# Kernel optimization log

Measured on AMD Instinct MI355X. Metric: run time of the kernel, lower is better.

The kernel has to match this reference:

```python
import jax, jax.numpy as jnp
import numpy as np

B, S, D, E, K = 4, 2048, 768, 8, 2


def setup_inputs() -> dict:
    key = jax.random.key(0)
    ks = jax.random.split(key, 5)
    s = 0.02
    return {
        "x": jax.random.normal(ks[0], (B, S, D), dtype=jnp.float32),
        "gate_w": jax.random.normal(ks[1], (D, E), dtype=jnp.float32) * s,
        "gate_b": jnp.zeros((E,), dtype=jnp.float32),
        "w1": jax.random.normal(ks[2], (E, D, D), dtype=jnp.float32) * s,
        "b1": jnp.zeros((E, D), dtype=jnp.float32),
        "w2": jax.random.normal(ks[3], (E, D, D), dtype=jnp.float32) * s,
        "b2": jnp.zeros((E, D), dtype=jnp.float32),
    }


def reference(x, gate_w, gate_b, w1, b1, w2, b2):
    # MoE forward, eval mode (no gate noise, dropout = identity)
    b, s, d = x.shape
    xf = x.reshape(-1, d)                                  # [T, D]
    T = xf.shape[0]

    gate_logits = xf @ gate_w + gate_b                     # [T, E]
    gate_scores = jax.nn.softmax(gate_logits, axis=-1)

    topv, topi = jax.lax.top_k(gate_scores, K)             # [T, K]
    topv = topv / (jnp.sum(topv, axis=-1, keepdims=True) + 1e-8)

    # scatter top-k weights into dense per-expert combine weights [T, E]
    comb = jnp.zeros((T, E), dtype=xf.dtype).at[
        jnp.arange(T)[:, None], topi].add(topv)

    # expert MLPs (dense over experts; combine weights zero-out unselected)
    h = jax.nn.relu(jnp.einsum('td,edh->teh', xf, w1) + b1)  # [T, E, D]
    y = jnp.einsum('teh,eho->teo', h, w2) + b2               # [T, E, D]
    out = jnp.einsum('te,teo->to', comb, y).reshape(b, s, -1)

    # load-balance aux loss (CV^2 of expert importance)
    importance = gate_scores.sum(axis=0)                   # [E]
    cv2 = importance.var() / (importance.mean() ** 2 + 1e-8)
    aux_loss = 0.01 * cv2
    return out, aux_loss
```

## Files before the change

kernel.cpp:

```cpp
#include <hip/hip_runtime.h>


#define T_TOK 8192
#define D_DIM 768
#define E_EXP 8
#define TK    16384
#define MAXCHUNK 136

typedef __attribute__((ext_vector_type(4))) float f32x4;
typedef __attribute__((ext_vector_type(8))) short s16x8;
typedef __attribute__((ext_vector_type(8))) unsigned short u16x8;

static __device__ __forceinline__ unsigned short f2bf(float f) {
    union { float f; unsigned u; } v; v.f = f;
    unsigned r = v.u + 0x7FFFu + ((v.u >> 16) & 1u);
    return (unsigned short)(r >> 16);
}
static __device__ __forceinline__ float bf2f(unsigned short h) {
    union { unsigned u; float f; } v; v.u = ((unsigned)h) << 16;
    return v.f;
}

static __device__ __forceinline__ void gload_lds16(const unsigned short* g, unsigned short* l) {
    __builtin_amdgcn_global_load_lds(
        (const __attribute__((address_space(1))) unsigned int*)(const void*)g,
        (__attribute__((address_space(3))) unsigned int*)(void*)l,
        16, 0, 0);
}

__global__ __launch_bounds__(256) void gate_kernel(
    const float* __restrict__ x, const float* __restrict__ gw,
    const float* __restrict__ gb, unsigned short* __restrict__ xb,
    int* __restrict__ ea, int* __restrict__ eb,
    float* __restrict__ wa, float* __restrict__ wb,
    int* __restrict__ counts, float* __restrict__ importance,
    int* __restrict__ basep, int* __restrict__ cursor,
    int* __restrict__ done, float* __restrict__ aux_out,
    int* __restrict__ nchunks, int* __restrict__ c2e, int* __restrict__ c2m)
{
    __shared__ float s_imp[4][8];
    __shared__ int   s_cnt[4][8];
    const int tid = threadIdx.x, wid = tid >> 6, lane = tid & 63;
    const int wg = blockIdx.x * 4 + wid;

    float imp[8]; int cnt[8];
    #pragma unroll
    for (int e = 0; e < 8; ++e) { imp[e] = 0.f; cnt[e] = 0; }

    for (int i = 0; i < 8; ++i) {
        const int t = wg + i * 1024;
        const float* xr = x + (size_t)t * D_DIM;
        float xv[12];
        float acc[8];
        #pragma unroll
        for (int e = 0; e < 8; ++e) acc[e] = 0.f;
        #pragma unroll
        for (int j = 0; j < 12; ++j) {
            const int d = lane + j * 64;
            float v = xr[d];
            xv[j] = v;
            xb[(size_t)t * D_DIM + d] = f2bf(v);
        }
        #pragma unroll
        for (int j = 0; j < 12; ++j) {
            const int d = lane + j * 64;
            const f32x4* g = (const f32x4*)(gw + (size_t)d * 8);
            f32x4 g0 = g[0], g1 = g[1];
            float v = xv[j];
            acc[0] += v * g0[0]; acc[1] += v * g0[1];
            acc[2] += v * g0[2]; acc[3] += v * g0[3];
            acc[4] += v * g1[0]; acc[5] += v * g1[1];
            acc[6] += v * g1[2]; acc[7] += v * g1[3];
        }
        #pragma unroll
        for (int s = 1; s < 64; s <<= 1) {
            #pragma unroll
            for (int e = 0; e < 8; ++e) acc[e] += __shfl_xor(acc[e], s);
        }
        float lg[8], mx = -1e30f;
        #pragma unroll
        for (int e = 0; e < 8; ++e) { lg[e] = acc[e] + gb[e]; mx = fmaxf(mx, lg[e]); }
        float p[8], ssum = 0.f;
        #pragma unroll
        for (int e = 0; e < 8; ++e) { p[e] = expf(lg[e] - mx); ssum += p[e]; }
        float sc[8];
        float inv_s = 1.f / ssum;
        #pragma unroll
        for (int e = 0; e < 8; ++e) { sc[e] = p[e] * inv_s; imp[e] += sc[e]; }
        float v0 = sc[0], v1 = -1e30f;
        int   i0 = 0,     i1 = -1;
        #pragma unroll
        for (int e = 1; e < 8; ++e) {
            if (sc[e] > v0)      { v1 = v0; i1 = i0; v0 = sc[e]; i0 = e; }
            else if (sc[e] > v1) { v1 = sc[e]; i1 = e; }
        }
        #pragma unroll
        for (int e = 0; e < 8; ++e) cnt[e] += (e == i0 ? 1 : 0) + (e == i1 ? 1 : 0);
        float inv = 1.f / (v0 + v1 + 1e-8f);
        if (lane == 0) {
            ea[t] = i0; eb[t] = i1; wa[t] = v0 * inv; wb[t] = v1 * inv;
        }
    }
    if (lane == 0) {
        #pragma unroll
        for (int e = 0; e < 8; ++e) { s_imp[wid][e] = imp[e]; s_cnt[wid][e] = cnt[e]; }
    }
    __syncthreads();
    if (tid < 8) {
        float si = 0.f; int sc2 = 0;
        #pragma unroll
        for (int w = 0; w < 4; ++w) { si += s_imp[w][tid]; sc2 += s_cnt[w][tid]; }
        atomicAdd(importance + tid, si);
        atomicAdd(counts + tid, sc2);
    }
    __threadfence();
    __syncthreads();
    if (tid == 0) {
        if (atomicAdd(done, 1) == (int)gridDim.x - 1) {
            int c[8]; float im[8];
            #pragma unroll
            for (int e = 0; e < 8; ++e) {
                c[e]  = atomicAdd(counts + e, 0);
                im[e] = atomicAdd(importance + e, 0.0f);
            }
            int b = 0, nc = 0;
            #pragma unroll
            for (int e = 0; e < 8; ++e) {
                basep[e] = b; cursor[e] = b;
                for (int m = 0; m < c[e]; m += 128) { c2e[nc] = e; c2m[nc] = m; ++nc; }
                b += c[e];
            }
            nchunks[0] = nc;
            float mean = 0.f;
            #pragma unroll
            for (int e = 0; e < 8; ++e) mean += im[e];
            mean *= 0.125f;
            float var = 0.f;
            #pragma unroll
            for (int e = 0; e < 8; ++e) { float d = im[e] - mean; var += d * d; }
            var *= 0.125f;
            aux_out[0] = 0.01f * var / (mean * mean + 1e-8f);
        }
    }
}

__global__ __launch_bounds__(256) void scatter_kernel(
    const int* __restrict__ ea, const int* __restrict__ eb,
    const float* __restrict__ wa, const float* __restrict__ wb,
    int* __restrict__ cursor, int* __restrict__ list,
    float* __restrict__ wgt, int* __restrict__ slot)
{
    const int t = blockIdx.x * 256 + threadIdx.x;
    const int lane = threadIdx.x & 63;
    #pragma unroll
    for (int k = 0; k < 2; ++k) {
        const int e = k ? eb[t] : ea[t];
        const float w = k ? wb[t] : wa[t];
        int pos = 0;
        for (int ex = 0; ex < 8; ++ex) {
            unsigned long long m = __ballot(e == ex);
            if (e == ex) {
                int leader = __ffsll((unsigned long long)m) - 1;
                int n = __popcll(m);
                int p0 = 0;
                if (lane == leader) p0 = atomicAdd(cursor + ex, n);
                p0 = __shfl(p0, leader);
                pos = p0 + __popcll(m & ((1ull << lane) - 1ull));
            }
        }
        list[pos] = t; wgt[pos] = w; slot[t * 2 + k] = pos;
    }
}

__global__ __launch_bounds__(256) void tconv_kernel(
    const float* __restrict__ w1, const float* __restrict__ w2,
    unsigned short* __restrict__ w1t, unsigned short* __restrict__ w2t)
{
    const int z = blockIdx.z;
    const float* src = (z < 8 ? w1 : w2) + (size_t)(z & 7) * D_DIM * D_DIM;
    unsigned short* dst = (z < 8 ? w1t : w2t) + (size_t)(z & 7) * D_DIM * D_DIM;
    __shared__ float tile[32][33];
    const int tx = threadIdx.x, ty = threadIdx.y;
    const int k0 = blockIdx.x * 32, n0 = blockIdx.y * 32;
    #pragma unroll
    for (int j = 0; j < 4; ++j)
        tile[ty + j * 8][tx] = src[(size_t)(k0 + ty + j * 8) * D_DIM + n0 + tx];
    __syncthreads();
    #pragma unroll
    for (int j = 0; j < 4; ++j)
        dst[(size_t)(n0 + ty + j * 8) * D_DIM + k0 + tx] = f2bf(tile[tx][ty + j * 8]);
}

template<int GATHER, int RELU>
__global__ __launch_bounds__(256) void moe_gemm_kernel(
    const unsigned short* __restrict__ A, const unsigned short* __restrict__ Bt,
    const float* __restrict__ bias, unsigned short* __restrict__ C,
    const int* __restrict__ counts, const int* __restrict__ basep,
    const int* __restrict__ list,
    const int* __restrict__ nchunks, const int* __restrict__ c2e,
    const int* __restrict__ c2m)
{
    const int cid = blockIdx.x;
    if (cid >= nchunks[0]) return;
    const int e = c2e[cid];
    const int m0 = c2m[cid];
    const int count = counts[e];
    const int n0 = blockIdx.y * 128;
    const int base = basep[e];

    constexpr int NT = D_DIM / 32;
    constexpr int LB = 128 * 32;

    __shared__ unsigned short Al[3 * LB];
    __shared__ unsigned short Bl[3 * LB];

    const int tid = threadIdx.x;
    const int lane = tid & 63, wid = tid >> 6;
    const int wr = wid >> 1, wc = wid & 1;

    const int sr = wid * 16 + (lane >> 2);
    const int sc = (lane & 3) * 8;

    int r0 = m0 + sr;      if (r0 >= count) r0 = count - 1;
    int r1 = m0 + 64 + sr; if (r1 >= count) r1 = count - 1;
    const size_t t0 = GATHER ? (size_t)list[base + r0] : (size_t)(base + r0);
    const size_t t1 = GATHER ? (size_t)list[base + r1] : (size_t)(base + r1);
    const unsigned short* gA0 = A + t0 * D_DIM + sc;
    const unsigned short* gA1 = A + t1 * D_DIM + sc;
    const unsigned short* gB0 = Bt + ((size_t)e * D_DIM + n0 + sr) * D_DIM + sc;
    const unsigned short* gB1 = Bt + ((size_t)e * D_DIM + n0 + 64 + sr) * D_DIM + sc;
    const int lds0 = (wid * 16) * 32;
    const int lds1 = (64 + wid * 16) * 32;

    f32x4 acc[4][4];
    #pragma unroll
    for (int mi = 0; mi < 4; ++mi)
        #pragma unroll
        for (int ni = 0; ni < 4; ++ni)
            acc[mi][ni] = (f32x4)(0.f);

#define STAGE(kt, bi) do {                                   \
        const int _k = (kt) * 32;                            \
        gload_lds16(gA0 + _k, Al + (bi) * LB + lds0);        \
        gload_lds16(gA1 + _k, Al + (bi) * LB + lds1);        \
        gload_lds16(gB0 + _k, Bl + (bi) * LB + lds0);        \
        gload_lds16(gB1 + _k, Bl + (bi) * LB + lds1);        \
    } while (0)

    STAGE(0, 0);
    STAGE(1, 1);
    asm volatile("s_waitcnt vmcnt(4)" ::: "memory");
    __builtin_amdgcn_s_barrier();
    __builtin_amdgcn_sched_barrier(0);

    #pragma unroll
    for (int t = 0; t < NT; ++t) {
        const int cb = t % 3;
        const int sb = (t + 2) % 3;
        if (t + 2 < NT) STAGE(t + 2, sb);

        s16x8 af[4], bfr[4];
        #pragma unroll
        for (int mi = 0; mi < 4; ++mi)
            af[mi] = *(const s16x8*)&Al[cb * LB + (wr * 64 + mi * 16 + (lane & 15)) * 32 + (lane >> 4) * 8];
        #pragma unroll
        for (int ni = 0; ni < 4; ++ni)
            bfr[ni] = *(const s16x8*)&Bl[cb * LB + (wc * 64 + ni * 16 + (lane & 15)) * 32 + (lane >> 4) * 8];
        #pragma unroll
        for (int mi = 0; mi < 4; ++mi)
            #pragma unroll
            for (int ni = 0; ni < 4; ++ni)
                acc[mi][ni] = __builtin_amdgcn_mfma_f32_16x16x32_bf16(
                    af[mi], bfr[ni], acc[mi][ni], 0, 0, 0);

        __builtin_amdgcn_sched_barrier(0);
        if (t + 2 < NT) { asm volatile("s_waitcnt vmcnt(4)" ::: "memory"); }
        else            { asm volatile("s_waitcnt vmcnt(0)" ::: "memory"); }
        __builtin_amdgcn_s_barrier();
        __builtin_amdgcn_sched_barrier(0);
    }
#undef STAGE

    #pragma unroll
    for (int ni = 0; ni < 4; ++ni) {
        const int cn = n0 + wc * 64 + ni * 16 + (lane & 15);
        const float bv = bias[e * D_DIM + cn];
        #pragma unroll
        for (int mi = 0; mi < 4; ++mi) {
            #pragma unroll
            for (int j = 0; j < 4; ++j) {
                const int rm = m0 + wr * 64 + mi * 16 + (lane >> 4) * 4 + j;
                if (rm < count) {
                    float v = acc[mi][ni][j] + bv;
                    if (RELU) v = fmaxf(v, 0.f);
                    C[(size_t)(base + rm) * D_DIM + cn] = f2bf(v);
                }
            }
        }
    }
}

__global__ __launch_bounds__(256) void combine_kernel(
    const unsigned short* __restrict__ y, const int* __restrict__ slot,
    const float* __restrict__ wgt, float* __restrict__ out)
{
    const int g = blockIdx.x * 256 + threadIdx.x;
    const int t = g / 96;
    const int n = (g % 96) * 8;
    const int s0 = slot[t * 2], s1 = slot[t * 2 + 1];
    const float w0 = wgt[s0], w1 = wgt[s1];
    u16x8 ya = *(const u16x8*)(y + (size_t)s0 * D_DIM + n);
    u16x8 yb = *(const u16x8*)(y + (size_t)s1 * D_DIM + n);
    f32x4 o0, o1;
    #pragma unroll
    for (int i = 0; i < 4; ++i) o0[i] = w0 * bf2f(ya[i])     + w1 * bf2f(yb[i]);
    #pragma unroll
    for (int i = 0; i < 4; ++i) o1[i] = w0 * bf2f(ya[4 + i]) + w1 * bf2f(yb[4 + i]);
    float* op = out + (size_t)t * D_DIM + n;
    *(f32x4*)op       = o0;
    *(f32x4*)(op + 4) = o1;
}

extern "C" void kernel_launch(void* const* d_in, const int* in_sizes, int n_in,
                              void* d_out, int out_size, void* d_ws, size_t ws_size,
                              hipStream_t stream)
{
    const float* x  = (const float*)d_in[0];
    const float* gw = (const float*)d_in[1];
    const float* gb = (const float*)d_in[2];
    const float* w1 = (const float*)d_in[3];
    const float* b1 = (const float*)d_in[4];
    const float* w2 = (const float*)d_in[5];
    const float* b2 = (const float*)d_in[6];
    float* out = (float*)d_out;

    char* ws = (char*)d_ws;
    size_t off = 0;
    auto alloc = [&](size_t bytes) {
        char* p = ws + off; off += (bytes + 255) & ~(size_t)255; return p;
    };
    unsigned short* xb  = (unsigned short*)alloc((size_t)T_TOK * D_DIM * 2);
    unsigned short* w1t = (unsigned short*)alloc((size_t)E_EXP * D_DIM * D_DIM * 2);
    unsigned short* w2t = (unsigned short*)alloc((size_t)E_EXP * D_DIM * D_DIM * 2);
    unsigned short* h   = (unsigned short*)alloc((size_t)TK * D_DIM * 2);
    unsigned short* y   = (unsigned short*)alloc((size_t)TK * D_DIM * 2);
    int*   list = (int*)alloc(TK * 4);
    float* wgt  = (float*)alloc(TK * 4);
    int*   slot = (int*)alloc(TK * 4);
    int*   ea   = (int*)alloc(T_TOK * 4);
    int*   eb   = (int*)alloc(T_TOK * 4);
    float* wa   = (float*)alloc(T_TOK * 4);
    float* wb   = (float*)alloc(T_TOK * 4);
    int*   meta = (int*)alloc(2048);
    int*   counts  = meta;
    int*   basep   = meta + 8;
    int*   cursor  = meta + 16;
    int*   done    = meta + 24;
    int*   nchunks = meta + 25;
    float* importance = (float*)(meta + 26);
    int*   c2e     = meta + 34;
    int*   c2m     = meta + 34 + MAXCHUNK;

    hipMemsetAsync(meta, 0, 2048, stream);
    tconv_kernel<<<dim3(24, 24, 16), dim3(32, 8), 0, stream>>>(w1, w2, w1t, w2t);
    gate_kernel<<<256, 256, 0, stream>>>(x, gw, gb, xb, ea, eb, wa, wb, counts, importance,
                                         basep, cursor, done, out + (out_size - 1),
                                         nchunks, c2e, c2m);
    scatter_kernel<<<32, 256, 0, stream>>>(ea, eb, wa, wb, cursor, list, wgt, slot);
    moe_gemm_kernel<1, 1><<<dim3(MAXCHUNK, 6), 256, 0, stream>>>(xb, w1t, b1, h, counts, basep, list,
                                                                 nchunks, c2e, c2m);
    moe_gemm_kernel<0, 0><<<dim3(MAXCHUNK, 6), 256, 0, stream>>>(h, w2t, b2, y, counts, basep, list,
                                                                 nchunks, c2e, c2m);
    combine_kernel<<<3072, 256, 0, stream>>>(y, slot, wgt, out);
}
```

Measured before the change: 296.2 us.

## Enlarge MoE GEMM M-tile to 256 with swizzled LDS and double gate grid

The expert GEMM tile grows from 128x128 to 256x128 rows per block. Each wave now holds 8x4 accumulators, and the chunk size and chunk count change to match. LDS reads use an XOR swizzle on the k-chunk to reduce bank conflicts, and the final-iteration barrier is dropped. The gate kernel launches twice as many blocks with fewer tokens each, for more parallelism. The larger tile roughly doubles accumulator register pressure (launch bounds ask for 2 blocks/SM) and leaves fewer blocks in the grid, with more padding waste on partial chunks.

```diff
diff --git a/kernel.cpp b/kernel.cpp
--- a/kernel.cpp
+++ b/kernel.cpp
@@ -5,7 +5,7 @@
 #define D_DIM 768
 #define E_EXP 8
 #define TK    16384
-#define MAXCHUNK 136
+#define MAXCHUNK 72
 
 typedef __attribute__((ext_vector_type(4))) float f32x4;
 typedef __attribute__((ext_vector_type(8))) short s16x8;
@@ -47,8 +47,8 @@
     #pragma unroll
     for (int e = 0; e < 8; ++e) { imp[e] = 0.f; cnt[e] = 0; }
 
-    for (int i = 0; i < 8; ++i) {
-        const int t = wg + i * 1024;
+    for (int i = 0; i < 4; ++i) {
+        const int t = wg + i * 2048;
         const float* xr = x + (size_t)t * D_DIM;
         float xv[12];
         float acc[8];
@@ -127,7 +127,7 @@
             #pragma unroll
             for (int e = 0; e < 8; ++e) {
                 basep[e] = b; cursor[e] = b;
-                for (int m = 0; m < c[e]; m += 128) { c2e[nc] = e; c2m[nc] = m; ++nc; }
+                for (int m = 0; m < c[e]; m += 256) { c2e[nc] = e; c2m[nc] = m; ++nc; }
                 b += c[e];
             }
             nchunks[0] = nc;
@@ -192,7 +192,7 @@
 }
 
 template<int GATHER, int RELU>
-__global__ __launch_bounds__(256) void moe_gemm_kernel(
+__global__ __launch_bounds__(256, 2) void moe_gemm_kernel(
     const unsigned short* __restrict__ A, const unsigned short* __restrict__ Bt,
     const float* __restrict__ bias, unsigned short* __restrict__ C,
     const int* __restrict__ counts, const int* __restrict__ basep,
@@ -208,88 +208,99 @@
     const int n0 = blockIdx.y * 128;
     const int base = basep[e];
 
-    constexpr int NT = D_DIM / 32;
-    constexpr int LB = 128 * 32;
-
-    __shared__ unsigned short Al[3 * LB];
-    __shared__ unsigned short Bl[3 * LB];
+    constexpr int NT  = D_DIM / 32;
+    constexpr int ALB = 256 * 32;
+    constexpr int BLB = 128 * 32;
+
+    __shared__ unsigned short Al[3 * ALB];
+    __shared__ unsigned short Bl[3 * BLB];
 
     const int tid = threadIdx.x;
     const int lane = tid & 63, wid = tid >> 6;
     const int wr = wid >> 1, wc = wid & 1;
 
-    const int sr = wid * 16 + (lane >> 2);
-    const int sc = (lane & 3) * 8;
-
-    int r0 = m0 + sr;      if (r0 >= count) r0 = count - 1;
-    int r1 = m0 + 64 + sr; if (r1 >= count) r1 = count - 1;
-    const size_t t0 = GATHER ? (size_t)list[base + r0] : (size_t)(base + r0);
-    const size_t t1 = GATHER ? (size_t)list[base + r1] : (size_t)(base + r1);
-    const unsigned short* gA0 = A + t0 * D_DIM + sc;
-    const unsigned short* gA1 = A + t1 * D_DIM + sc;
-    const unsigned short* gB0 = Bt + ((size_t)e * D_DIM + n0 + sr) * D_DIM + sc;
-    const unsigned short* gB1 = Bt + ((size_t)e * D_DIM + n0 + 64 + sr) * D_DIM + sc;
-    const int lds0 = (wid * 16) * 32;
-    const int lds1 = (64 + wid * 16) * 32;
-
-    f32x4 acc[4][4];
-    #pragma unroll
-    for (int mi = 0; mi < 4; ++mi)
+    const int ro  = lane >> 2;
+    const int sch = ((lane & 3) ^ (ro & 3)) * 8;
+
+    const unsigned short *gA0, *gA1, *gA2, *gA3, *gB0, *gB1;
+    {
+        int r, row;
+        row = wid * 64 + 0 * 16 + ro; r = m0 + row; if (r >= count) r = count - 1;
+        gA0 = A + (GATHER ? (size_t)list[base + r] : (size_t)(base + r)) * D_DIM + sch;
+        row = wid * 64 + 1 * 16 + ro; r = m0 + row; if (r >= count) r = count - 1;
+        gA1 = A + (GATHER ? (size_t)list[base + r] : (size_t)(base + r)) * D_DIM + sch;
+        row = wid * 64 + 2 * 16 + ro; r = m0 + row; if (r >= count) r = count - 1;
+        gA2 = A + (GATHER ? (size_t)list[base + r] : (size_t)(base + r)) * D_DIM + sch;
+        row = wid * 64 + 3 * 16 + ro; r = m0 + row; if (r >= count) r = count - 1;
+        gA3 = A + (GATHER ? (size_t)list[base + r] : (size_t)(base + r)) * D_DIM + sch;
+        gB0 = Bt + ((size_t)e * D_DIM + n0 + wid * 32 + 0 * 16 + ro) * D_DIM + sch;
+        gB1 = Bt + ((size_t)e * D_DIM + n0 + wid * 32 + 1 * 16 + ro) * D_DIM + sch;
+    }
+    const int lA0 = (wid * 64 +  0) * 32, lA1 = (wid * 64 + 16) * 32;
+    const int lA2 = (wid * 64 + 32) * 32, lA3 = (wid * 64 + 48) * 32;
+    const int lB0 = (wid * 32 +  0) * 32, lB1 = (wid * 32 + 16) * 32;
+
+#define STAGE(kt, bi) do {                                      \
+        gload_lds16(gA0 + (kt) * 32, Al + (bi) * ALB + lA0);    \
+        gload_lds16(gA1 + (kt) * 32, Al + (bi) * ALB + lA1);    \
+        gload_lds16(gA2 + (kt) * 32, Al + (bi) * ALB + lA2);    \
+        gload_lds16(gA3 + (kt) * 32, Al + (bi) * ALB + lA3);    \
+        gload_lds16(gB0 + (kt) * 32, Bl + (bi) * BLB + lB0);    \
+        gload_lds16(gB1 + (kt) * 32, Bl + (bi) * BLB + lB1);    \
+    } while (0)
+
+    f32x4 acc[8][4];
+    #pragma unroll
+    for (int mi = 0; mi < 8; ++mi)
         #pragma unroll
         for (int ni = 0; ni < 4; ++ni)
             acc[mi][ni] = (f32x4)(0.f);
 
-#define STAGE(kt, bi) do {                                   \
-        const int _k = (kt) * 32;                            \
-        gload_lds16(gA0 + _k, Al + (bi) * LB + lds0);        \
-        gload_lds16(gA1 + _k, Al + (bi) * LB + lds1);        \
-        gload_lds16(gB0 + _k, Bl + (bi) * LB + lds0);        \
-        gload_lds16(gB1 + _k, Bl + (bi) * LB + lds1);        \
-    } while (0)
+    const int sw8 = (((lane >> 4) ^ (lane & 3)) * 8);
+    const int l15 = lane & 15;
 
     STAGE(0, 0);
     STAGE(1, 1);
-    asm volatile("s_waitcnt vmcnt(4)" ::: "memory");
+    asm volatile("s_waitcnt vmcnt(6)" ::: "memory");
     __builtin_amdgcn_s_barrier();
     __builtin_amdgcn_sched_barrier(0);
 
     #pragma unroll
     for (int t = 0; t < NT; ++t) {
         const int cb = t % 3;
-        const int sb = (t + 2) % 3;
-        if (t + 2 < NT) STAGE(t + 2, sb);
-
-        s16x8 af[4], bfr[4];
-        #pragma unroll
-        for (int mi = 0; mi < 4; ++mi)
-            af[mi] = *(const s16x8*)&Al[cb * LB + (wr * 64 + mi * 16 + (lane & 15)) * 32 + (lane >> 4) * 8];
+        if (t + 2 < NT) STAGE(t + 2, (t + 2) % 3);
+
+        s16x8 af[8], bfr[4];
+        #pragma unroll
+        for (int mi = 0; mi < 8; ++mi)
+            af[mi] = *(const s16x8*)&Al[cb * ALB + (wr * 128 + mi * 16 + l15) * 32 + sw8];
         #pragma unroll
         for (int ni = 0; ni < 4; ++ni)
-            bfr[ni] = *(const s16x8*)&Bl[cb * LB + (wc * 64 + ni * 16 + (lane & 15)) * 32 + (lane >> 4) * 8];
-        #pragma unroll
-        for (int mi = 0; mi < 4; ++mi)
+            bfr[ni] = *(const s16x8*)&Bl[cb * BLB + (wc * 64 + ni * 16 + l15) * 32 + sw8];
+        #pragma unroll
+        for (int mi = 0; mi < 8; ++mi)
             #pragma unroll
             for (int ni = 0; ni < 4; ++ni)
                 acc[mi][ni] = __builtin_amdgcn_mfma_f32_16x16x32_bf16(
                     af[mi], bfr[ni], acc[mi][ni], 0, 0, 0);
 
         __builtin_amdgcn_sched_barrier(0);
-        if (t + 2 < NT) { asm volatile("s_waitcnt vmcnt(4)" ::: "memory"); }
+        if (t < NT - 2) { asm volatile("s_waitcnt vmcnt(6)" ::: "memory"); }
         else            { asm volatile("s_waitcnt vmcnt(0)" ::: "memory"); }
-        __builtin_amdgcn_s_barrier();
+        if (t < NT - 1) __builtin_amdgcn_s_barrier();
         __builtin_amdgcn_sched_barrier(0);
     }
 #undef STAGE
 
     #pragma unroll
     for (int ni = 0; ni < 4; ++ni) {
-        const int cn = n0 + wc * 64 + ni * 16 + (lane & 15);
+        const int cn = n0 + wc * 64 + ni * 16 + l15;
         const float bv = bias[e * D_DIM + cn];
         #pragma unroll
-        for (int mi = 0; mi < 4; ++mi) {
+        for (int mi = 0; mi < 8; ++mi) {
             #pragma unroll
             for (int j = 0; j < 4; ++j) {
-                const int rm = m0 + wr * 64 + mi * 16 + (lane >> 4) * 4 + j;
+                const int rm = m0 + wr * 128 + mi * 16 + (lane >> 4) * 4 + j;
                 if (rm < count) {
                     float v = acc[mi][ni][j] + bv;
                     if (RELU) v = fmaxf(v, 0.f);
@@ -363,7 +374,7 @@
 
     hipMemsetAsync(meta, 0, 2048, stream);
     tconv_kernel<<<dim3(24, 24, 16), dim3(32, 8), 0, stream>>>(w1, w2, w1t, w2t);
-    gate_kernel<<<256, 256, 0, stream>>>(x, gw, gb, xb, ea, eb, wa, wb, counts, importance,
+    gate_kernel<<<512, 256, 0, stream>>>(x, gw, gb, xb, ea, eb, wa, wb, counts, importance,
                                          basep, cursor, done, out + (out_size - 1),
                                          nchunks, c2e, c2m);
     scatter_kernel<<<32, 256, 0, stream>>>(ea, eb, wa, wb, cursor, list, wgt, slot);
```

Result: no change. 300.4 us (+1.4%).
